# Performance work log

Measured on AMD Instinct MI355X. Metric: run time of the kernel, lower is better.

Reference implementation:

```python
import jax, jax.numpy as jnp
import numpy as np

N_NODES = 100000
N_EDGES = 1600000
D_FEAT = 64
HIDDEN = 64


def _glorot(key, shape):
    fan_in, fan_out = shape[1], shape[0]
    limit = float(np.sqrt(6.0 / (fan_in + fan_out)))
    return jax.random.uniform(key, shape, jnp.float32, -limit, limit)


def setup_inputs() -> dict:
    key = jax.random.key(0)
    ks = jax.random.split(key, 8)
    x = jax.random.normal(ks[0], (N_NODES, D_FEAT), jnp.float32)
    edge_index = jax.random.randint(ks[1], (2, N_EDGES), 0, N_NODES, jnp.int64)
    # SAGEConv params: lin_l applied to aggregated neighbors (has bias),
    # lin_r applied to root/self features (no bias in PyG default).
    params = {
        "W1_l": _glorot(ks[2], (HIDDEN, D_FEAT)),
        "b1": jnp.zeros((HIDDEN,), jnp.float32),
        "W1_r": _glorot(ks[3], (HIDDEN, D_FEAT)),
        "W2_l": _glorot(ks[4], (HIDDEN, HIDDEN)),
        "b2": jnp.zeros((HIDDEN,), jnp.float32),
        "W2_r": _glorot(ks[5], (HIDDEN, HIDDEN)),
    }
    return {"x": x, "edge_index": edge_index, **params}


def _sage_conv(x, src, dst, deg_inv, W_l, b, W_r):
    # mean-aggregate neighbor features: gather at src, segment-sum at dst
    msg = jax.ops.segment_sum(x[src], dst, num_segments=N_NODES)  # [N, F]
    agg = msg * deg_inv[:, None]
    return agg @ W_l.T + b + x @ W_r.T


def reference(x, edge_index, W1_l, b1, W1_r, W2_l, b2, W2_r):
    src, dst = edge_index[0], edge_index[1]
    deg = jax.ops.segment_sum(jnp.ones((N_EDGES,), x.dtype), dst,
                              num_segments=N_NODES)
    deg_inv = 1.0 / jnp.maximum(deg, 1.0)  # PyG mean clamps count to >=1
    h = jax.nn.relu(_sage_conv(x, src, dst, deg_inv, W1_l, b1, W1_r))
    out = _sage_conv(h, src, dst, deg_inv, W2_l, b2, W2_r)
    return out
```

## Files before the change

### kernel.cpp

```cpp
#include <hip/hip_runtime.h>
#include <hip/hip_bf16.h>

#define FEAT 64

typedef __bf16 bf16x8 __attribute__((ext_vector_type(8)));
typedef __bf16 bf16x4 __attribute__((ext_vector_type(4)));
typedef float  f32x4  __attribute__((ext_vector_type(4)));

__global__ __launch_bounds__(256)
void zero2_kernel(int* __restrict__ a, int* __restrict__ b, int n) {
    int i = blockIdx.x * 256 + threadIdx.x;
    if (i < n) { a[i] = 0; b[i] = 0; }
}

__global__ void detect_idx_kernel(const unsigned* __restrict__ w, int* __restrict__ flag,
                                  int* __restrict__ zcnt) {
    __shared__ int any_nz;
    if (threadIdx.x == 0) any_nz = 0;
    __syncthreads();
    if (w[2 * threadIdx.x + 1] != 0u) atomicOr(&any_nz, 1);
    zcnt[threadIdx.x] = 0;
    zcnt[threadIdx.x + 256] = 0;
    __syncthreads();
    if (threadIdx.x == 0) *flag = (any_nz == 0) ? 1 : 0;
}

__device__ __forceinline__ int load_idx_clamped(const void* ei, long long i, int is64, int n_nodes) {
    int v = is64 ? ((const int*)ei)[2 * i] : ((const int*)ei)[i];
    v = v < 0 ? 0 : v;
    return v >= n_nodes ? n_nodes - 1 : v;
}


__global__ __launch_bounds__(256)
void bucket_count_kernel(const void* __restrict__ ei, const int* __restrict__ flagp,
                         int* __restrict__ gcnt, int n_edges, int n_nodes) {
    __shared__ int cnt[512];
    const int t = threadIdx.x;
    cnt[t] = 0; cnt[t + 256] = 0;
    __syncthreads();
    const int is64 = *flagp;
    for (int e = blockIdx.x * 256 + t; e < n_edges; e += gridDim.x * 256) {
        int d = load_idx_clamped(ei, (long long)n_edges + e, is64, n_nodes);
        atomicAdd(&cnt[d >> 9], 1);
    }
    __syncthreads();
    if (cnt[t])       atomicAdd(&gcnt[t], cnt[t]);
    if (cnt[t + 256]) atomicAdd(&gcnt[t + 256], cnt[t + 256]);
}

__global__ void bucket_scan_kernel(const int* __restrict__ gcnt, int* __restrict__ gbase,
                                   int* __restrict__ gcur, int n_edges) {
    __shared__ int sh[512];
    int t = threadIdx.x;
    int v = gcnt[t];
    sh[t] = v;
    __syncthreads();
    for (int off = 1; off < 512; off <<= 1) {
        int u = (t >= off) ? sh[t - off] : 0;
        __syncthreads();
        sh[t] += u;
        __syncthreads();
    }
    int excl = sh[t] - v;
    gbase[t] = excl;
    gcur[t]  = excl;
    if (t == 511) gbase[512] = n_edges;
}

__global__ __launch_bounds__(256)
void multisplit_kernel(const void* __restrict__ ei, const int* __restrict__ flagp,
                       int* __restrict__ gcur, unsigned* __restrict__ B,
                       int n_edges, int n_nodes) {
    __shared__ unsigned sv[4096];
    __shared__ unsigned dv[4096];
    __shared__ int cnt[512];
    __shared__ int cur[512];
    const int t = threadIdx.x;
    const int is64 = *flagp;
    const int ntiles = (n_edges + 4095) >> 12;
    for (int tile = blockIdx.x; tile < ntiles; tile += gridDim.x) {
        cnt[t] = 0; cnt[t + 256] = 0;
        __syncthreads();
        #pragma unroll
        for (int k = 0; k < 16; ++k) {
            int i = k * 256 + t;
            int e = (tile << 12) + i;
            unsigned dmark = 0xFFFFFFFFu, s = 0;
            if (e < n_edges) {
                s     = (unsigned)load_idx_clamped(ei, e, is64, n_nodes);
                int d = load_idx_clamped(ei, (long long)n_edges + e, is64, n_nodes);
                dmark = (unsigned)d;
                atomicAdd(&cnt[d >> 9], 1);
            }
            sv[i] = s; dv[i] = dmark;
        }
        __syncthreads();
        if (cnt[t])       cur[t]       = atomicAdd(&gcur[t], cnt[t]);
        if (cnt[t + 256]) cur[t + 256] = atomicAdd(&gcur[t + 256], cnt[t + 256]);
        __syncthreads();
        #pragma unroll
        for (int k = 0; k < 16; ++k) {
            int i = k * 256 + t;
            unsigned d = dv[i];
            if (d != 0xFFFFFFFFu) {
                int pos = atomicAdd(&cur[d >> 9], 1);
                pos = pos < 0 ? 0 : (pos >= n_edges ? n_edges - 1 : pos);
                B[pos] = ((d & 511u) << 17) | sv[i];
            }
        }
        __syncthreads();
    }
}

__global__ __launch_bounds__(256)
void csr_build2_kernel(const unsigned* __restrict__ B, const int* __restrict__ gbase,
                       int* __restrict__ degc, int* __restrict__ offs,
                       float* __restrict__ dinv, int* __restrict__ csr,
                       int n_edges, int n_nodes) {
    __shared__ int cnt[512];
    __shared__ int scn[512];
    __shared__ int cur[512];
    const int b = blockIdx.x, t = threadIdx.x;
    cnt[t] = 0; cnt[t + 256] = 0;
    __syncthreads();
    const int lo = gbase[b], hi = gbase[b + 1];
    for (int i = lo + t; i < hi; i += 256) {
        unsigned v = B[i];
        atomicAdd(&cnt[v >> 17], 1);
    }
    __syncthreads();
    scn[t] = cnt[t]; scn[t + 256] = cnt[t + 256];
    __syncthreads();
    for (int off = 1; off < 512; off <<= 1) {
        int u0 = (t >= off) ? scn[t - off] : 0;
        int u1 = (t + 256 >= off) ? scn[t + 256 - off] : 0;
        __syncthreads();
        scn[t] += u0; scn[t + 256] += u1;
        __syncthreads();
    }
    const int base = gbase[b];
    int e0 = base + scn[t] - cnt[t];
    int e1 = base + scn[t + 256] - cnt[t + 256];
    cur[t] = e0; cur[t + 256] = e1;
    int n0 = b * 512 + t, n1 = n0 + 256;
    if (n0 < n_nodes) {
        degc[n0] = cnt[t]; offs[n0] = e0;
        dinv[n0] = 1.0f / fmaxf((float)cnt[t], 1.0f);
    }
    if (n1 < n_nodes) {
        degc[n1] = cnt[t + 256]; offs[n1] = e1;
        dinv[n1] = 1.0f / fmaxf((float)cnt[t + 256], 1.0f);
    }
    __syncthreads();
    for (int i = lo + t; i < hi; i += 256) {
        unsigned v = B[i];
        int pos = atomicAdd(&cur[v >> 17], 1);
        pos = pos < 0 ? 0 : (pos >= n_edges ? n_edges - 1 : pos);
        csr[pos] = (int)(v & 0x1FFFFu);
    }
}

__global__ __launch_bounds__(256)
void scan_partial_kernel(const int* __restrict__ degc, int* __restrict__ part, int n_nodes) {
    __shared__ int sh[256];
    int i = blockIdx.x * 256 + threadIdx.x;
    sh[threadIdx.x] = (i < n_nodes) ? degc[i] : 0;
    __syncthreads();
    for (int off = 128; off > 0; off >>= 1) {
        if (threadIdx.x < off) sh[threadIdx.x] += sh[threadIdx.x + off];
        __syncthreads();
    }
    if (threadIdx.x == 0) part[blockIdx.x] = sh[0];
}

__global__ void scan_top_kernel(int* __restrict__ part, int nparts) {
    __shared__ int sh[512];
    int t = threadIdx.x;
    int v = (t < nparts) ? part[t] : 0;
    sh[t] = v;
    __syncthreads();
    for (int off = 1; off < 512; off <<= 1) {
        int u = (t >= off) ? sh[t - off] : 0;
        __syncthreads();
        sh[t] += u;
        __syncthreads();
    }
    if (t < nparts) part[t] = sh[t] - v;
}

__global__ __launch_bounds__(256)
void scan_final_kernel(const int* __restrict__ degc, const int* __restrict__ part,
                       int* __restrict__ offs, float* __restrict__ deg_inv, int n_nodes) {
    __shared__ int sh[256];
    int t = threadIdx.x;
    int i = blockIdx.x * 256 + t;
    int v = (i < n_nodes) ? degc[i] : 0;
    sh[t] = v;
    __syncthreads();
    for (int off = 1; off < 256; off <<= 1) {
        int u = (t >= off) ? sh[t - off] : 0;
        __syncthreads();
        sh[t] += u;
        __syncthreads();
    }
    if (i < n_nodes) {
        offs[i]    = sh[t] - v + part[blockIdx.x];
        deg_inv[i] = 1.0f / fmaxf((float)v, 1.0f);
    }
}

__global__ __launch_bounds__(256)
void hist_kernel(const void* __restrict__ ei, const int* __restrict__ flagp,
                 int* __restrict__ degc, int n_edges, int n_nodes) {
    int e = blockIdx.x * 256 + threadIdx.x;
    if (e >= n_edges) return;
    int d = load_idx_clamped(ei, (long long)n_edges + e, *flagp, n_nodes);
    atomicAdd(&degc[d], 1);
}

__global__ __launch_bounds__(256)
void csr_scatter_kernel(const void* __restrict__ ei, const int* __restrict__ flagp,
                        const int* __restrict__ offs, int* __restrict__ cursor,
                        int* __restrict__ csr, int n_edges, int n_nodes) {
    int e = blockIdx.x * 256 + threadIdx.x;
    if (e >= n_edges) return;
    int is64 = *flagp;
    int s = load_idx_clamped(ei, e, is64, n_nodes);
    int d = load_idx_clamped(ei, (long long)n_edges + e, is64, n_nodes);
    int pos = offs[d] + atomicAdd(&cursor[d], 1);
    pos = pos < 0 ? 0 : (pos >= n_edges ? n_edges - 1 : pos);
    csr[pos] = s;
}

__global__ __launch_bounds__(256)
void cast_w_kernel(const float* __restrict__ a, const float* __restrict__ b,
                   const float* __restrict__ c, const float* __restrict__ d,
                   __bf16* __restrict__ o) {
    int i = blockIdx.x * 256 + threadIdx.x;
    if (i < FEAT * FEAT) {
        o[i]         = (__bf16)a[i];
        o[4096 + i]  = (__bf16)b[i];
        o[8192 + i]  = (__bf16)c[i];
        o[12288 + i] = (__bf16)d[i];
    }
}

__global__ __launch_bounds__(256)
void cast_x_kernel(const float* __restrict__ x, __bf16* __restrict__ xb, int n4) {
    int i = blockIdx.x * 256 + threadIdx.x;
    if (i < n4) {
        float4 v = ((const float4*)x)[i];
        bf16x4 o;
        o.x = (__bf16)v.x; o.y = (__bf16)v.y; o.z = (__bf16)v.z; o.w = (__bf16)v.w;
        ((bf16x4*)xb)[i] = o;
    }
}

__global__ __launch_bounds__(256)
void gather_bf16_kernel(const __bf16* __restrict__ hin, const int* __restrict__ offs,
                        const int* __restrict__ degc, const float* __restrict__ dinv,
                        const int* __restrict__ csr, __bf16* __restrict__ agg,
                        int n_nodes) {
    const int t = threadIdx.x, lane = t & 63, g = lane >> 4, u = lane & 15;
    const int gw = blockIdx.x * 4 + (t >> 6), nw = gridDim.x * 4;
    if (gw >= n_nodes) return;
    int rs = offs[gw], cnt = degc[gw];
    float di = dinv[gw];
    int lim0 = cnt < 64 ? cnt : 64;
    int pf = (lane < lim0) ? (int)__builtin_nontemporal_load(&csr[rs + lane]) : 0;
    for (int n = gw; n < n_nodes; n += nw) {
        const int nn = n + nw;
        int rs2 = 0, cnt2 = 0;
        float di2 = 1.0f;
        if (nn < n_nodes) { rs2 = offs[nn]; cnt2 = degc[nn]; di2 = dinv[nn]; }
        float a0 = 0.f, a1 = 0.f, a2 = 0.f, a3 = 0.f;
        int myid = pf;
        int c = 0;
        while (true) {
            int chunk = cnt - c; chunk = chunk > 64 ? 64 : chunk;
            myid = myid < 0 ? 0 : (myid >= n_nodes ? n_nodes - 1 : myid);
            for (int q = 0; q < chunk; q += 16) {
                int q0 = q + g, q1 = q + g + 4, q2 = q + g + 8, q3 = q + g + 12;
                int s0 = __shfl(myid, q0);
                int s1 = __shfl(myid, q1);
                int s2 = __shfl(myid, q2);
                int s3 = __shfl(myid, q3);
                float m0 = (q0 < chunk) ? 1.f : 0.f;
                float m1 = (q1 < chunk) ? 1.f : 0.f;
                float m2 = (q2 < chunk) ? 1.f : 0.f;
                float m3 = (q3 < chunk) ? 1.f : 0.f;
                bf16x4 v0 = ((const bf16x4*)hin)[(size_t)s0 * 16 + u];
                bf16x4 v1 = ((const bf16x4*)hin)[(size_t)s1 * 16 + u];
                bf16x4 v2 = ((const bf16x4*)hin)[(size_t)s2 * 16 + u];
                bf16x4 v3 = ((const bf16x4*)hin)[(size_t)s3 * 16 + u];
                a0 = fmaf(m0, (float)v0.x, a0); a1 = fmaf(m0, (float)v0.y, a1);
                a2 = fmaf(m0, (float)v0.z, a2); a3 = fmaf(m0, (float)v0.w, a3);
                a0 = fmaf(m1, (float)v1.x, a0); a1 = fmaf(m1, (float)v1.y, a1);
                a2 = fmaf(m1, (float)v1.z, a2); a3 = fmaf(m1, (float)v1.w, a3);
                a0 = fmaf(m2, (float)v2.x, a0); a1 = fmaf(m2, (float)v2.y, a1);
                a2 = fmaf(m2, (float)v2.z, a2); a3 = fmaf(m2, (float)v2.w, a3);
                a0 = fmaf(m3, (float)v3.x, a0); a1 = fmaf(m3, (float)v3.y, a1);
                a2 = fmaf(m3, (float)v3.z, a2); a3 = fmaf(m3, (float)v3.w, a3);
            }
            c += 64;
            if (c >= cnt) break;
            int rem = cnt - c, lim = rem < 64 ? rem : 64;
            myid = (lane < lim) ? (int)__builtin_nontemporal_load(&csr[rs + c + lane]) : 0;
        }
        {
            int lim2 = cnt2 < 64 ? cnt2 : 64;
            pf = (nn < n_nodes && lane < lim2)
                     ? (int)__builtin_nontemporal_load(&csr[rs2 + lane]) : 0;
        }
        a0 += __shfl_xor(a0, 16); a1 += __shfl_xor(a1, 16);
        a2 += __shfl_xor(a2, 16); a3 += __shfl_xor(a3, 16);
        a0 += __shfl_xor(a0, 32); a1 += __shfl_xor(a1, 32);
        a2 += __shfl_xor(a2, 32); a3 += __shfl_xor(a3, 32);
        if (g == 0) {
            bf16x4 o;
            o.x = (__bf16)(a0 * di); o.y = (__bf16)(a1 * di);
            o.z = (__bf16)(a2 * di); o.w = (__bf16)(a3 * di);
            ((bf16x4*)agg)[(size_t)n * 16 + u] = o;
        }
        rs = rs2; cnt = cnt2; di = di2;
    }
}

__global__ __launch_bounds__(256)
void gather_f32_kernel(const float* __restrict__ xin, const int* __restrict__ offs,
                       const int* __restrict__ degc, const float* __restrict__ dinv,
                       const int* __restrict__ csr, __bf16* __restrict__ agg,
                       int n_nodes) {
    const int t = threadIdx.x, lane = t & 63, g = lane >> 4, u = lane & 15;
    const int gw = blockIdx.x * 4 + (t >> 6), nw = gridDim.x * 4;
    for (int n = gw; n < n_nodes; n += nw) {
        int rs = offs[n], cnt = degc[n];
        float a0 = 0.f, a1 = 0.f, a2 = 0.f, a3 = 0.f;
        for (int c = 0; c < cnt; c += 64) {
            int chunk = min(64, cnt - c);
            int myid = (lane < chunk) ? (int)__builtin_nontemporal_load(&csr[rs + c + lane]) : 0;
            myid = myid < 0 ? 0 : (myid >= n_nodes ? n_nodes - 1 : myid);
            for (int q = 0; q < chunk; q += 16) {
                int q0 = q + g, q1 = q + g + 4, q2 = q + g + 8, q3 = q + g + 12;
                int s0 = __shfl(myid, q0), s1 = __shfl(myid, q1);
                int s2 = __shfl(myid, q2), s3 = __shfl(myid, q3);
                float m0 = (q0 < chunk) ? 1.f : 0.f;
                float m1 = (q1 < chunk) ? 1.f : 0.f;
                float m2 = (q2 < chunk) ? 1.f : 0.f;
                float m3 = (q3 < chunk) ? 1.f : 0.f;
                float4 v0 = ((const float4*)xin)[(size_t)s0 * 16 + u];
                float4 v1 = ((const float4*)xin)[(size_t)s1 * 16 + u];
                float4 v2 = ((const float4*)xin)[(size_t)s2 * 16 + u];
                float4 v3 = ((const float4*)xin)[(size_t)s3 * 16 + u];
                a0 = fmaf(m0, v0.x, a0); a1 = fmaf(m0, v0.y, a1);
                a2 = fmaf(m0, v0.z, a2); a3 = fmaf(m0, v0.w, a3);
                a0 = fmaf(m1, v1.x, a0); a1 = fmaf(m1, v1.y, a1);
                a2 = fmaf(m1, v1.z, a2); a3 = fmaf(m1, v1.w, a3);
                a0 = fmaf(m2, v2.x, a0); a1 = fmaf(m2, v2.y, a1);
                a2 = fmaf(m2, v2.z, a2); a3 = fmaf(m2, v2.w, a3);
                a0 = fmaf(m3, v3.x, a0); a1 = fmaf(m3, v3.y, a1);
                a2 = fmaf(m3, v3.z, a2); a3 = fmaf(m3, v3.w, a3);
            }
        }
        a0 += __shfl_xor(a0, 16); a1 += __shfl_xor(a1, 16);
        a2 += __shfl_xor(a2, 16); a3 += __shfl_xor(a3, 16);
        a0 += __shfl_xor(a0, 32); a1 += __shfl_xor(a1, 32);
        a2 += __shfl_xor(a2, 32); a3 += __shfl_xor(a3, 32);
        if (g == 0) {
            float di = dinv[n];
            bf16x4 o;
            o.x = (__bf16)(a0 * di); o.y = (__bf16)(a1 * di);
            o.z = (__bf16)(a2 * di); o.w = (__bf16)(a3 * di);
            ((bf16x4*)agg)[(size_t)n * 16 + u] = o;
        }
    }
}

__global__ __launch_bounds__(256)
void gemm_l1b_kernel(const __bf16* __restrict__ Ag, const __bf16* __restrict__ xb,
                     const __bf16* __restrict__ Bl, const __bf16* __restrict__ Br,
                     const float* __restrict__ bias,
                     __bf16* __restrict__ hout, int n_nodes) {
    const int t = threadIdx.x, lane = t & 63;
    const int quad = lane >> 4, r16 = lane & 15;
    bf16x8 bl[2][4], br[2][4];
    #pragma unroll
    for (int ks = 0; ks < 2; ++ks)
        #pragma unroll
        for (int ct = 0; ct < 4; ++ct) {
            int f = ct * 16 + r16, k = ks * 32 + quad * 8;
            bl[ks][ct] = *(const bf16x8*)(Bl + f * 64 + k);
            br[ks][ct] = *(const bf16x8*)(Br + f * 64 + k);
        }
    const int m0 = (blockIdx.x * 4 + (t >> 6)) * 16;
    if (m0 >= n_nodes) return;
    int mrow = m0 + r16; if (mrow >= n_nodes) mrow = n_nodes - 1;
    bf16x8 ag[2], ax[2];
    #pragma unroll
    for (int ks = 0; ks < 2; ++ks) {
        ag[ks] = *(const bf16x8*)(Ag + (size_t)mrow * 64 + ks * 32 + quad * 8);
        ax[ks] = *(const bf16x8*)(xb + (size_t)mrow * 64 + ks * 32 + quad * 8);
    }
    #pragma unroll
    for (int ct = 0; ct < 4; ++ct) {
        f32x4 acc = {0.f, 0.f, 0.f, 0.f};
        acc = __builtin_amdgcn_mfma_f32_16x16x32_bf16(ag[0], bl[0][ct], acc, 0, 0, 0);
        acc = __builtin_amdgcn_mfma_f32_16x16x32_bf16(ag[1], bl[1][ct], acc, 0, 0, 0);
        acc = __builtin_amdgcn_mfma_f32_16x16x32_bf16(ax[0], br[0][ct], acc, 0, 0, 0);
        acc = __builtin_amdgcn_mfma_f32_16x16x32_bf16(ax[1], br[1][ct], acc, 0, 0, 0);
        int col = ct * 16 + r16;
        float bv = bias[col];
        #pragma unroll
        for (int rg = 0; rg < 4; ++rg) {
            int n = m0 + quad * 4 + rg;
            if (n < n_nodes) {
                float o = acc[rg] + bv;
                hout[(size_t)n * 64 + col] = (__bf16)fmaxf(o, 0.f);
            }
        }
    }
}

__global__ __launch_bounds__(256)
void gemm_l1_kernel(const __bf16* __restrict__ Ag, const float* __restrict__ xin,
                    const __bf16* __restrict__ Bl, const __bf16* __restrict__ Br,
                    const float* __restrict__ bias,
                    __bf16* __restrict__ hout, int n_nodes) {
    const int t = threadIdx.x, lane = t & 63;
    const int quad = lane >> 4, r16 = lane & 15;
    bf16x8 bl[2][4], br[2][4];
    #pragma unroll
    for (int ks = 0; ks < 2; ++ks)
        #pragma unroll
        for (int ct = 0; ct < 4; ++ct) {
            int f = ct * 16 + r16, k = ks * 32 + quad * 8;
            bl[ks][ct] = *(const bf16x8*)(Bl + f * 64 + k);
            br[ks][ct] = *(const bf16x8*)(Br + f * 64 + k);
        }
    const int m0 = (blockIdx.x * 4 + (t >> 6)) * 16;
    if (m0 >= n_nodes) return;
    int mrow = m0 + r16; if (mrow >= n_nodes) mrow = n_nodes - 1;
    bf16x8 ag[2], ax[2];
    #pragma unroll
    for (int ks = 0; ks < 2; ++ks) {
        ag[ks] = *(const bf16x8*)(Ag + (size_t)mrow * 64 + ks * 32 + quad * 8);
        const float* xr = xin + (size_t)mrow * 64 + ks * 32 + quad * 8;
        float4 p = *(const float4*)xr;
        float4 q = *(const float4*)(xr + 4);
        union { bf16x8 v; __bf16 e[8]; } U;
        U.e[0] = (__bf16)p.x; U.e[1] = (__bf16)p.y; U.e[2] = (__bf16)p.z; U.e[3] = (__bf16)p.w;
        U.e[4] = (__bf16)q.x; U.e[5] = (__bf16)q.y; U.e[6] = (__bf16)q.z; U.e[7] = (__bf16)q.w;
        ax[ks] = U.v;
    }
    #pragma unroll
    for (int ct = 0; ct < 4; ++ct) {
        f32x4 acc = {0.f, 0.f, 0.f, 0.f};
        acc = __builtin_amdgcn_mfma_f32_16x16x32_bf16(ag[0], bl[0][ct], acc, 0, 0, 0);
        acc = __builtin_amdgcn_mfma_f32_16x16x32_bf16(ag[1], bl[1][ct], acc, 0, 0, 0);
        acc = __builtin_amdgcn_mfma_f32_16x16x32_bf16(ax[0], br[0][ct], acc, 0, 0, 0);
        acc = __builtin_amdgcn_mfma_f32_16x16x32_bf16(ax[1], br[1][ct], acc, 0, 0, 0);
        int col = ct * 16 + r16;
        float bv = bias[col];
        #pragma unroll
        for (int rg = 0; rg < 4; ++rg) {
            int n = m0 + quad * 4 + rg;
            if (n < n_nodes) {
                float o = acc[rg] + bv;
                hout[(size_t)n * 64 + col] = (__bf16)fmaxf(o, 0.f);
            }
        }
    }
}

__global__ __launch_bounds__(256)
void gemm_l2_kernel(const __bf16* __restrict__ Ag, const __bf16* __restrict__ Ah,
                    const __bf16* __restrict__ Bl, const __bf16* __restrict__ Br,
                    const float* __restrict__ bias,
                    float* __restrict__ out, int n_nodes) {
    const int t = threadIdx.x, lane = t & 63;
    const int quad = lane >> 4, r16 = lane & 15;
    bf16x8 bl[2][4], br[2][4];
    #pragma unroll
    for (int ks = 0; ks < 2; ++ks)
        #pragma unroll
        for (int ct = 0; ct < 4; ++ct) {
            int f = ct * 16 + r16, k = ks * 32 + quad * 8;
            bl[ks][ct] = *(const bf16x8*)(Bl + f * 64 + k);
            br[ks][ct] = *(const bf16x8*)(Br + f * 64 + k);
        }
    const int m0 = (blockIdx.x * 4 + (t >> 6)) * 16;
    if (m0 >= n_nodes) return;
    int mrow = m0 + r16; if (mrow >= n_nodes) mrow = n_nodes - 1;
    bf16x8 ag[2], ah[2];
    #pragma unroll
    for (int ks = 0; ks < 2; ++ks) {
        ag[ks] = *(const bf16x8*)(Ag + (size_t)mrow * 64 + ks * 32 + quad * 8);
        ah[ks] = *(const bf16x8*)(Ah + (size_t)mrow * 64 + ks * 32 + quad * 8);
    }
    #pragma unroll
    for (int ct = 0; ct < 4; ++ct) {
        f32x4 acc = {0.f, 0.f, 0.f, 0.f};
        acc = __builtin_amdgcn_mfma_f32_16x16x32_bf16(ag[0], bl[0][ct], acc, 0, 0, 0);
        acc = __builtin_amdgcn_mfma_f32_16x16x32_bf16(ag[1], bl[1][ct], acc, 0, 0, 0);
        acc = __builtin_amdgcn_mfma_f32_16x16x32_bf16(ah[0], br[0][ct], acc, 0, 0, 0);
        acc = __builtin_amdgcn_mfma_f32_16x16x32_bf16(ah[1], br[1][ct], acc, 0, 0, 0);
        int col = ct * 16 + r16;
        float bv = bias[col];
        #pragma unroll
        for (int rg = 0; rg < 4; ++rg) {
            int n = m0 + quad * 4 + rg;
            if (n < n_nodes) out[(size_t)n * 64 + col] = acc[rg] + bv;
        }
    }
}

__global__ __launch_bounds__(256)
void sage_fused_l1_kernel(const float* __restrict__ xin,
                          const int* __restrict__ offs, const int* __restrict__ degc,
                          const float* __restrict__ deg_inv, const int* __restrict__ csr,
                          const float* __restrict__ Wl, const float* __restrict__ bias,
                          const float* __restrict__ Wr,
                          __bf16* __restrict__ hout, int n_nodes) {
    __shared__ float WlT[FEAT * 65], WrT[FEAT * 65], bsh[FEAT];
    __shared__ float aggS[4][FEAT], selfS[4][FEAT];
    const int t = threadIdx.x;
    #pragma unroll
    for (int p = 0; p < 16; ++p) {
        int i = t + p * 256, j = i >> 6, k = i & 63;
        WlT[k * 65 + j] = Wl[i];
        WrT[k * 65 + j] = Wr[i];
    }
    if (t < FEAT) bsh[t] = bias[t];
    __syncthreads();
    const int w = t >> 6, f = t & 63;
    const int n_groups = (n_nodes + 3) >> 2;
    for (int g = blockIdx.x; g < n_groups; g += gridDim.x) {
        int n = g * 4 + w;
        bool act = (n < n_nodes);
        if (act) {
            int rs = offs[n], cnt = degc[n];
            float acc = 0.f;
            for (int c = 0; c < cnt; c += 64) {
                int chunk = min(64, cnt - c);
                int myid = (f < chunk) ? csr[rs + c + f] : 0;
                #pragma unroll 4
                for (int q = 0; q < chunk; ++q) {
                    int s = __shfl(myid, q);
                    acc += xin[(long long)s * FEAT + f];
                }
            }
            aggS[w][f]  = acc * deg_inv[n];
            selfS[w][f] = xin[(long long)n * FEAT + f];
        }
        __syncthreads();
        if (act) {
            float o = bsh[f];
            #pragma unroll
            for (int k = 0; k < FEAT; ++k) {
                o = fmaf(aggS[w][k],  WlT[k * 65 + f], o);
                o = fmaf(selfS[w][k], WrT[k * 65 + f], o);
            }
            o = fmaxf(o, 0.f);
            hout[(long long)n * FEAT + f] = (__bf16)o;
        }
        __syncthreads();
    }
}

__global__ __launch_bounds__(256)
void sage_fused_l2_kernel(const __bf16* __restrict__ hin,
                          const int* __restrict__ offs, const int* __restrict__ degc,
                          const float* __restrict__ deg_inv, const int* __restrict__ csr,
                          const float* __restrict__ Wl, const float* __restrict__ bias,
                          const float* __restrict__ Wr,
                          float* __restrict__ out, int n_nodes) {
    __shared__ float WlT[FEAT * 65], WrT[FEAT * 65], bsh[FEAT];
    __shared__ float aggS[4][FEAT], selfS[4][FEAT];
    const int t = threadIdx.x;
    #pragma unroll
    for (int p = 0; p < 16; ++p) {
        int i = t + p * 256, j = i >> 6, k = i & 63;
        WlT[k * 65 + j] = Wl[i];
        WrT[k * 65 + j] = Wr[i];
    }
    if (t < FEAT) bsh[t] = bias[t];
    __syncthreads();
    const int w = t >> 6, f = t & 63;
    const int n_groups = (n_nodes + 3) >> 2;
    for (int g = blockIdx.x; g < n_groups; g += gridDim.x) {
        int n = g * 4 + w;
        bool act = (n < n_nodes);
        if (act) {
            int rs = offs[n], cnt = degc[n];
            float acc = 0.f;
            for (int c = 0; c < cnt; c += 64) {
                int chunk = min(64, cnt - c);
                int myid = (f < chunk) ? csr[rs + c + f] : 0;
                #pragma unroll 4
                for (int q = 0; q < chunk; ++q) {
                    int s = __shfl(myid, q);
                    acc += (float)hin[(long long)s * FEAT + f];
                }
            }
            aggS[w][f]  = acc * deg_inv[n];
            selfS[w][f] = (float)hin[(long long)n * FEAT + f];
        }
        __syncthreads();
        if (act) {
            float o = bsh[f];
            #pragma unroll
            for (int k = 0; k < FEAT; ++k) {
                o = fmaf(aggS[w][k],  WlT[k * 65 + f], o);
                o = fmaf(selfS[w][k], WrT[k * 65 + f], o);
            }
            out[(long long)n * FEAT + f] = o;
        }
        __syncthreads();
    }
}

extern "C" void kernel_launch(void* const* d_in, const int* in_sizes, int n_in,
                              void* d_out, int out_size, void* d_ws, size_t ws_size,
                              hipStream_t stream) {
    const float* x   = (const float*)d_in[0];
    const void*  ei  = d_in[1];
    const float* W1l = (const float*)d_in[2];
    const float* b1  = (const float*)d_in[3];
    const float* W1r = (const float*)d_in[4];
    const float* W2l = (const float*)d_in[5];
    const float* b2  = (const float*)d_in[6];
    const float* W2r = (const float*)d_in[7];
    float* out = (float*)d_out;

    const int n_nodes = in_sizes[0] / FEAT;
    const int n_edges = in_sizes[1] / 2;
    const int nparts  = (n_nodes + 255) / 256;
    const int egrid   = (n_edges + 255) / 256;
    const int NB      = (n_nodes + 511) >> 9;

    char* ws = (char*)d_ws;
    auto al = [](size_t v) { return (v + 255) & ~(size_t)255; };

    size_t o = 0;
    int*      flag  = (int*)(ws + o);      o += 256;
    int*      degc  = (int*)(ws + o);      o += al((size_t)n_nodes * 4);
    float*    dinv  = (float*)(ws + o);    o += al((size_t)n_nodes * 4);
    int*      offs  = (int*)(ws + o);      o += al((size_t)n_nodes * 4);
    int*      gcnt  = (int*)(ws + o);      o += al(512 * 4);
    int*      gbase = (int*)(ws + o);      o += al(513 * 4);
    int*      gcur  = (int*)(ws + o);      o += al(512 * 4);
    unsigned* B     = (unsigned*)(ws + o); o += al((size_t)n_edges * 4);
    int*      csr   = (int*)(ws + o);      o += al((size_t)n_edges * 4);
    __bf16*   xb    = (__bf16*)(ws + o);   o += al((size_t)n_nodes * FEAT * 2);
    __bf16*   wb    = (__bf16*)(ws + o);   o += al((size_t)4 * FEAT * FEAT * 2);
    __bf16*   agg   = (__bf16*)(ws + o);   o += al((size_t)n_nodes * FEAT * 2);
    __bf16*   h     = (__bf16*)(ws + o);   o += al((size_t)n_nodes * FEAT * 2);
    const size_t needT1 = o;

    size_t o3 = 0;
    int*    flag3   = (int*)(ws + o3);    o3 += 256;
    int*    degc3   = (int*)(ws + o3);    o3 += al((size_t)n_nodes * 4);
    float*  dinv3   = (float*)(ws + o3);  o3 += al((size_t)n_nodes * 4);
    int*    offs3   = (int*)(ws + o3);    o3 += al((size_t)n_nodes * 4);
    int*    cursor3 = (int*)(ws + o3);    o3 += al((size_t)n_nodes * 4);
    int*    part3   = (int*)(ws + o3);    o3 += al(2048);
    int*    csr3    = (int*)(ws + o3);    o3 += al((size_t)n_edges * 4);
    const size_t commonEnd3 = o3;
    __bf16* wb3  = (__bf16*)(ws + o3);    o3 += al((size_t)4 * FEAT * FEAT * 2);
    __bf16* agg3 = (__bf16*)(ws + o3);    o3 += al((size_t)n_nodes * FEAT * 2);
    __bf16* h3   = (__bf16*)(ws + o3);    o3 += al((size_t)n_nodes * FEAT * 2);
    const size_t needT3 = o3;

    const int n4 = n_nodes * FEAT / 4;
    const int mgrid = (n_nodes + 63) / 64;
    const int ggrid = 2048;
    const int ntiles = (n_edges + 4095) >> 12;

    if (ws_size >= needT1 && n_nodes <= 131072) {
        detect_idx_kernel<<<1, 256, 0, stream>>>((const unsigned*)ei, flag, gcnt);
        bucket_count_kernel<<<512, 256, 0, stream>>>(ei, flag, gcnt, n_edges, n_nodes);
        bucket_scan_kernel<<<1, 512, 0, stream>>>(gcnt, gbase, gcur, n_edges);
        multisplit_kernel<<<ntiles, 256, 0, stream>>>(ei, flag, gcur, B, n_edges, n_nodes);
        cast_x_kernel<<<(n4 + 255) / 256, 256, 0, stream>>>(x, xb, n4);
        cast_w_kernel<<<16, 256, 0, stream>>>(W1l, W1r, W2l, W2r, wb);
        csr_build2_kernel<<<NB, 256, 0, stream>>>(B, gbase, degc, offs, dinv, csr, n_edges, n_nodes);
        gather_bf16_kernel<<<ggrid, 256, 0, stream>>>(xb, offs, degc, dinv, csr, agg, n_nodes);
        gemm_l1b_kernel<<<mgrid, 256, 0, stream>>>(agg, xb, wb, wb + 4096, b1, h, n_nodes);
        gather_bf16_kernel<<<ggrid, 256, 0, stream>>>(h, offs, degc, dinv, csr, agg, n_nodes);
        gemm_l2_kernel<<<mgrid, 256, 0, stream>>>(agg, h, wb + 8192, wb + 12288, b2, out, n_nodes);
    } else if (ws_size >= needT3) {
        zero2_kernel<<<nparts, 256, 0, stream>>>(degc3, cursor3, n_nodes);
        detect_idx_kernel<<<1, 256, 0, stream>>>((const unsigned*)ei, flag3, part3);
        hist_kernel<<<egrid, 256, 0, stream>>>(ei, flag3, degc3, n_edges, n_nodes);
        scan_partial_kernel<<<nparts, 256, 0, stream>>>(degc3, part3, n_nodes);
        scan_top_kernel<<<1, 512, 0, stream>>>(part3, nparts);
        scan_final_kernel<<<nparts, 256, 0, stream>>>(degc3, part3, offs3, dinv3, n_nodes);
        csr_scatter_kernel<<<egrid, 256, 0, stream>>>(ei, flag3, offs3, cursor3, csr3, n_edges, n_nodes);
        cast_w_kernel<<<16, 256, 0, stream>>>(W1l, W1r, W2l, W2r, wb3);
        gather_f32_kernel<<<ggrid, 256, 0, stream>>>(x, offs3, degc3, dinv3, csr3, agg3, n_nodes);
        gemm_l1_kernel<<<mgrid, 256, 0, stream>>>(agg3, x, wb3, wb3 + 4096, b1, h3, n_nodes);
        gather_bf16_kernel<<<ggrid, 256, 0, stream>>>(h3, offs3, degc3, dinv3, csr3, agg3, n_nodes);
        gemm_l2_kernel<<<mgrid, 256, 0, stream>>>(agg3, h3, wb3 + 8192, wb3 + 12288, b2, out, n_nodes);
    } else {
        __bf16* hf = (__bf16*)(ws + commonEnd3);
        zero2_kernel<<<nparts, 256, 0, stream>>>(degc3, cursor3, n_nodes);
        detect_idx_kernel<<<1, 256, 0, stream>>>((const unsigned*)ei, flag3, part3);
        hist_kernel<<<egrid, 256, 0, stream>>>(ei, flag3, degc3, n_edges, n_nodes);
        scan_partial_kernel<<<nparts, 256, 0, stream>>>(degc3, part3, n_nodes);
        scan_top_kernel<<<1, 512, 0, stream>>>(part3, nparts);
        scan_final_kernel<<<nparts, 256, 0, stream>>>(degc3, part3, offs3, dinv3, n_nodes);
        csr_scatter_kernel<<<egrid, 256, 0, stream>>>(ei, flag3, offs3, cursor3, csr3, n_edges, n_nodes);
        const int n_groups = (n_nodes + 3) / 4;
        const int fgrid = n_groups < 4096 ? n_groups : 4096;
        sage_fused_l1_kernel<<<fgrid, 256, 0, stream>>>(x, offs3, degc3, dinv3, csr3,
                                                        W1l, b1, W1r, hf, n_nodes);
        sage_fused_l2_kernel<<<fgrid, 256, 0, stream>>>(hf, offs3, degc3, dinv3, csr3,
                                                        W2l, b2, W2r, out, n_nodes);
    }
}
```

Baseline: 266.5 us.

## Assign one 16-lane group per node in bf16 gather instead of one wave

The bf16 neighbor-gather kernel now gives each node to a 16-lane group, so a wave handles four nodes at once, instead of one 64-lane wave per node with cross-group shuffle reductions. Each group loads 16 neighbor indices, issues 16 independent row loads per chunk, and writes its result directly, with no xor-shuffle reduction. This cuts idle lanes for low-degree nodes (average degree about 16) and raises memory-level parallelism. The cost is more register pressure from the 16-element load arrays, and wasted masked loads when a node's degree is not a multiple of 16.

Measured after the change: 267.7 us. About the same (+0.5%).

```diff
diff --git a/kernel.cpp b/kernel.cpp
--- a/kernel.cpp
+++ b/kernel.cpp
@@ -262,67 +262,47 @@
                         const int* __restrict__ degc, const float* __restrict__ dinv,
                         const int* __restrict__ csr, __bf16* __restrict__ agg,
                         int n_nodes) {
-    const int t = threadIdx.x, lane = t & 63, g = lane >> 4, u = lane & 15;
-    const int gw = blockIdx.x * 4 + (t >> 6), nw = gridDim.x * 4;
-    if (gw >= n_nodes) return;
-    int rs = offs[gw], cnt = degc[gw];
-    float di = dinv[gw];
-    int lim0 = cnt < 64 ? cnt : 64;
-    int pf = (lane < lim0) ? (int)__builtin_nontemporal_load(&csr[rs + lane]) : 0;
-    for (int n = gw; n < n_nodes; n += nw) {
-        const int nn = n + nw;
+    const int t = threadIdx.x, u = t & 15;
+    const int g0 = blockIdx.x * 16 + (t >> 4);
+    const int ng = gridDim.x * 16;
+    if (g0 >= n_nodes) return;
+    int rs = offs[g0], cnt = degc[g0];
+    float di = dinv[g0];
+    int idx = (u < cnt) ? (int)__builtin_nontemporal_load(&csr[rs + u]) : 0;
+    for (int n = g0; n < n_nodes; n += ng) {
+        const int nn = n + ng;
         int rs2 = 0, cnt2 = 0;
         float di2 = 1.0f;
         if (nn < n_nodes) { rs2 = offs[nn]; cnt2 = degc[nn]; di2 = dinv[nn]; }
         float a0 = 0.f, a1 = 0.f, a2 = 0.f, a3 = 0.f;
-        int myid = pf;
         int c = 0;
         while (true) {
-            int chunk = cnt - c; chunk = chunk > 64 ? 64 : chunk;
-            myid = myid < 0 ? 0 : (myid >= n_nodes ? n_nodes - 1 : myid);
-            for (int q = 0; q < chunk; q += 16) {
-                int q0 = q + g, q1 = q + g + 4, q2 = q + g + 8, q3 = q + g + 12;
-                int s0 = __shfl(myid, q0);
-                int s1 = __shfl(myid, q1);
-                int s2 = __shfl(myid, q2);
-                int s3 = __shfl(myid, q3);
-                float m0 = (q0 < chunk) ? 1.f : 0.f;
-                float m1 = (q1 < chunk) ? 1.f : 0.f;
-                float m2 = (q2 < chunk) ? 1.f : 0.f;
-                float m3 = (q3 < chunk) ? 1.f : 0.f;
-                bf16x4 v0 = ((const bf16x4*)hin)[(size_t)s0 * 16 + u];
-                bf16x4 v1 = ((const bf16x4*)hin)[(size_t)s1 * 16 + u];
-                bf16x4 v2 = ((const bf16x4*)hin)[(size_t)s2 * 16 + u];
-                bf16x4 v3 = ((const bf16x4*)hin)[(size_t)s3 * 16 + u];
-                a0 = fmaf(m0, (float)v0.x, a0); a1 = fmaf(m0, (float)v0.y, a1);
-                a2 = fmaf(m0, (float)v0.z, a2); a3 = fmaf(m0, (float)v0.w, a3);
-                a0 = fmaf(m1, (float)v1.x, a0); a1 = fmaf(m1, (float)v1.y, a1);
-                a2 = fmaf(m1, (float)v1.z, a2); a3 = fmaf(m1, (float)v1.w, a3);
-                a0 = fmaf(m2, (float)v2.x, a0); a1 = fmaf(m2, (float)v2.y, a1);
-                a2 = fmaf(m2, (float)v2.z, a2); a3 = fmaf(m2, (float)v2.w, a3);
-                a0 = fmaf(m3, (float)v3.x, a0); a1 = fmaf(m3, (float)v3.y, a1);
-                a2 = fmaf(m3, (float)v3.z, a2); a3 = fmaf(m3, (float)v3.w, a3);
-            }
-            c += 64;
+            idx = idx < 0 ? 0 : (idx >= n_nodes ? n_nodes - 1 : idx);
+            int sj[16];
+            #pragma unroll
+            for (int j = 0; j < 16; ++j) sj[j] = __shfl(idx, j, 16);
+            bf16x4 v[16];
+            #pragma unroll
+            for (int j = 0; j < 16; ++j)
+                v[j] = ((const bf16x4*)hin)[(size_t)sj[j] * 16 + u];
+            #pragma unroll
+            for (int j = 0; j < 16; ++j) {
+                float m = (c + j < cnt) ? 1.f : 0.f;
+                a0 = fmaf(m, (float)v[j].x, a0);
+                a1 = fmaf(m, (float)v[j].y, a1);
+                a2 = fmaf(m, (float)v[j].z, a2);
+                a3 = fmaf(m, (float)v[j].w, a3);
+            }
+            c += 16;
             if (c >= cnt) break;
-            int rem = cnt - c, lim = rem < 64 ? rem : 64;
-            myid = (lane < lim) ? (int)__builtin_nontemporal_load(&csr[rs + c + lane]) : 0;
-        }
-        {
-            int lim2 = cnt2 < 64 ? cnt2 : 64;
-            pf = (nn < n_nodes && lane < lim2)
-                     ? (int)__builtin_nontemporal_load(&csr[rs2 + lane]) : 0;
-        }
-        a0 += __shfl_xor(a0, 16); a1 += __shfl_xor(a1, 16);
-        a2 += __shfl_xor(a2, 16); a3 += __shfl_xor(a3, 16);
-        a0 += __shfl_xor(a0, 32); a1 += __shfl_xor(a1, 32);
-        a2 += __shfl_xor(a2, 32); a3 += __shfl_xor(a3, 32);
-        if (g == 0) {
-            bf16x4 o;
-            o.x = (__bf16)(a0 * di); o.y = (__bf16)(a1 * di);
-            o.z = (__bf16)(a2 * di); o.w = (__bf16)(a3 * di);
-            ((bf16x4*)agg)[(size_t)n * 16 + u] = o;
-        }
+            idx = (u < cnt - c) ? (int)__builtin_nontemporal_load(&csr[rs + c + u]) : 0;
+        }
+        idx = (nn < n_nodes && u < cnt2)
+                  ? (int)__builtin_nontemporal_load(&csr[rs2 + u]) : 0;
+        bf16x4 o;
+        o.x = (__bf16)(a0 * di); o.y = (__bf16)(a1 * di);
+        o.z = (__bf16)(a2 * di); o.w = (__bf16)(a3 * di);
+        ((bf16x4*)agg)[(size_t)n * 16 + u] = o;
         rs = rs2; cnt = cnt2; di = di2;
     }
 }
```
